# Kernel tuning notes

Hardware: AMD Instinct MI355X
Metric: run time of the kernel (lower is better)

## Reference

```python
import jax, jax.numpy as jnp
import numpy as np

D = 20                 # input_dim
N = 1_000_000          # batch
NC = 2 ** (D + 1)      # number of dummy expert Linear(1,1) modules


def setup_inputs() -> dict:
    key = jax.random.key(0)
    ks = jax.random.split(key, 12)
    x = jax.random.randint(ks[0], (N, D), 0, 2).astype(jnp.float32)   # binary features
    t = jax.random.randint(ks[1], (N, 1), 0, 2).astype(jnp.float32)   # binary treatment
    y = jax.random.normal(ks[2], (N, 1), dtype=jnp.float32)           # outcome fed to dummy linears
    # Encoder dummy experts: one (w, b) pair per combination of (t, x)
    qz_w = jax.random.normal(ks[3], (NC,), dtype=jnp.float32) * 0.1
    qz_b = jax.random.normal(ks[4], (NC,), dtype=jnp.float32) * 0.1
    # Decoder per-feature Linear(1,1) for binary x
    dx_w = jax.random.normal(ks[5], (D,), dtype=jnp.float32) * 0.1
    dx_b = jax.random.normal(ks[6], (D,), dtype=jnp.float32) * 0.1
    # Decoder scalar Linear(1,1) heads
    t_w = jax.random.normal(ks[7], (), dtype=jnp.float32) * 0.1
    t_b = jnp.zeros((), jnp.float32)
    y0_w = jax.random.normal(ks[8], (), dtype=jnp.float32) * 0.1
    y0_b = jnp.zeros((), jnp.float32)
    y1_w = jax.random.normal(ks[9], (), dtype=jnp.float32) * 0.1
    y1_b = jnp.zeros((), jnp.float32)
    pz_logit = jnp.zeros((1,), jnp.float32)
    return {"x": x, "t": t, "y": y, "qz_w": qz_w, "qz_b": qz_b,
            "dx_w": dx_w, "dx_b": dx_b, "t_w": t_w, "t_b": t_b,
            "y0_w": y0_w, "y0_b": y0_b, "y1_w": y1_w, "y1_b": y1_b,
            "pz_logit": pz_logit}


def _combo_index(x, t):
    # itertools.product([0,1], repeat=D+1): combs[i][0] is the t bit (MSB),
    # combs[i][1:] are the x bits, so i = t*2^D + sum_j x_j * 2^(D-1-j).
    pow2 = (2 ** jnp.arange(D - 1, -1, -1)).astype(jnp.int32)   # [D]
    return t[:, 0].astype(jnp.int32) * (2 ** D) + x.astype(jnp.int32) @ pow2  # [N]


def _decode(z, t, dx_w, dx_b, t_w, t_b, y0_w, y0_b, y1_w, y1_b):
    # Vectorized form of per-feature Linear(1,1) loops: x_logits[:, i] = w_i*z + b_i
    x_logits = z * dx_w[None, :] + dx_b[None, :]          # [N, D]
    t_logits = z * t_w + t_b                              # [N, 1]
    y_logits = (z * y1_w + y1_b) * t + (z * y0_w + y0_b) * (1.0 - t)  # [N, 1]
    return x_logits, t_logits, y_logits


def reference(x, t, y, qz_w, qz_b, dx_w, dx_b, t_w, t_b,
              y0_w, y0_b, y1_w, y1_b, pz_logit):
    # Encoder (z_mode='binary'): sum over all 2^(D+1) experts of
    # (w_i*y + b_i) * onehot_mask_i == gather by combination index (inputs binary).
    idx = _combo_index(x, t)                                  # [N]
    z_logits = (qz_w[idx] * y[:, 0] + qz_b[idx])[:, None]     # [N, 1]
    n = x.shape[0]
    z0 = jnp.zeros((n, 1), jnp.float32)
    z1 = jnp.ones((n, 1), jnp.float32)
    x_logits0, t_logits0, y_logits0 = _decode(z0, t, dx_w, dx_b, t_w, t_b, y0_w, y0_b, y1_w, y1_b)
    x_logits1, t_logits1, y_logits1 = _decode(z1, t, dx_w, dx_b, t_w, t_b, y0_w, y0_b, y1_w, y1_b)
    return (z_logits, x_logits0, x_logits1, t_logits0, t_logits1,
            y_logits0, y_logits1, pz_logit)
```

## Files before the change

kernel.cpp:

```cpp
#include <hip/hip_runtime.h>

constexpr int D = 20;

typedef float f4 __attribute__((ext_vector_type(4)));
typedef unsigned int u32;

__device__ __forceinline__ u32 bf16_rne(float f) {
    u32 u = __float_as_uint(f);
    return (u + 0x7FFFu + ((u >> 16) & 1u)) >> 16;
}

__global__ __launch_bounds__(256) void cevae_build_tab(
    const f4* __restrict__ qw, const f4* __restrict__ qb,
    uint4* __restrict__ tab, int nq)
{
    int i = blockIdx.x * 256 + threadIdx.x;
    if (i >= nq) return;
    f4 w = qw[i];
    f4 b = qb[i];
    uint4 o;
    o.x = (bf16_rne(w.x) << 16) | bf16_rne(b.x);
    o.y = (bf16_rne(w.y) << 16) | bf16_rne(b.y);
    o.z = (bf16_rne(w.z) << 16) | bf16_rne(b.z);
    o.w = (bf16_rne(w.w) << 16) | bf16_rne(b.w);
    tab[i] = o;
}

template <bool USE_TAB>
__global__ __launch_bounds__(256) void cevae_fused7_kernel(
    const float* __restrict__ x, const float* __restrict__ t,
    const float* __restrict__ y, const u32* __restrict__ tab,
    const float* __restrict__ qz_w, const float* __restrict__ qz_b,
    const float* __restrict__ dx_w, const float* __restrict__ dx_b,
    const float* __restrict__ sc_tw, const float* __restrict__ sc_tb,
    const float* __restrict__ sc_y0w, const float* __restrict__ sc_y0b,
    const float* __restrict__ sc_y1w, const float* __restrict__ sc_y1b,
    const float* __restrict__ pz, float* __restrict__ out, int n_rows,
    int n_job_blocks)
{
    int bid = blockIdx.x;
    int sub = ((bid >> 4) << 3) | (bid & 7);
    size_t o3 = (size_t)n_rows * (size_t)(1 + 2 * D);

    if (((bid >> 3) & 1) == 0) {
        int n = sub * 256 + threadIdx.x;
        if (n >= n_rows) return;

        const f4* xr = (const f4*)(x + (size_t)n * D);
        f4 a = xr[0];
        f4 b = xr[1];
        f4 c = xr[2];
        f4 d = xr[3];
        f4 e = xr[4];
        float tv = t[n];
        float yv = y[n];

        unsigned idx = (tv != 0.0f) ? (1u << 20) : 0u;
        idx |= ((unsigned)a.x) << 19;
        idx |= ((unsigned)a.y) << 18;
        idx |= ((unsigned)a.z) << 17;
        idx |= ((unsigned)a.w) << 16;
        idx |= ((unsigned)b.x) << 15;
        idx |= ((unsigned)b.y) << 14;
        idx |= ((unsigned)b.z) << 13;
        idx |= ((unsigned)b.w) << 12;
        idx |= ((unsigned)c.x) << 11;
        idx |= ((unsigned)c.y) << 10;
        idx |= ((unsigned)c.z) << 9;
        idx |= ((unsigned)c.w) << 8;
        idx |= ((unsigned)d.x) << 7;
        idx |= ((unsigned)d.y) << 6;
        idx |= ((unsigned)d.z) << 5;
        idx |= ((unsigned)d.w) << 4;
        idx |= ((unsigned)e.x) << 3;
        idx |= ((unsigned)e.y) << 2;
        idx |= ((unsigned)e.z) << 1;
        idx |= ((unsigned)e.w);

        float z;
        if (USE_TAB) {
            u32 g = tab[idx];
            z = fmaf(__uint_as_float(g & 0xFFFF0000u), yv,
                     __uint_as_float(g << 16));
        } else {
            z = fmaf(qz_w[idx], yv, qz_b[idx]);
        }
        out[n] = z;

        float y0w = *sc_y0w, y0b = *sc_y0b;
        float y1w = *sc_y1w, y1b = *sc_y1b;

        out[o3 + 2 * (size_t)n_rows + n] = fmaf(tv, y1b - y0b, y0b);
        out[o3 + 3 * (size_t)n_rows + n] = fmaf(tv, (y1w + y1b) - (y0w + y0b), y0w + y0b);
        if (n == 0) out[o3 + 4 * (size_t)n_rows] = pz[0];
    } else {
        unsigned Q = (unsigned)n_rows * D / 4;
        f4* r0 = (f4*)(out + n_rows);
        f4* r1 = r0 + Q;
        unsigned stride = (unsigned)n_job_blocks * 256;
        unsigned q0 = (unsigned)sub * 256 + threadIdx.x;
        for (unsigned q = q0; q < Q; q += stride) {
            int cb = (int)(q % 5u) * 4;
            float b0 = dx_b[cb + 0], b1 = dx_b[cb + 1];
            float b2 = dx_b[cb + 2], b3 = dx_b[cb + 3];
            float w0 = dx_w[cb + 0], w1 = dx_w[cb + 1];
            float w2 = dx_w[cb + 2], w3 = dx_w[cb + 3];
            f4 v0 = {b0, b1, b2, b3};
            f4 v1 = {w0 + b0, w1 + b1, w2 + b2, w3 + b3};
            __builtin_nontemporal_store(v0, r0 + q);
            __builtin_nontemporal_store(v1, r1 + q);
        }
        float tw = *sc_tw, tb = *sc_tb;
        f4 s0 = {tb, tb, tb, tb};
        float t1v = tw + tb;
        f4 s1 = {t1v, t1v, t1v, t1v};
        unsigned Qt = (unsigned)n_rows / 4;
        f4* h0 = (f4*)(out + o3);
        f4* h1 = (f4*)(out + o3 + (size_t)n_rows);
        for (unsigned q = q0; q < Qt; q += stride) {
            __builtin_nontemporal_store(s0, h0 + q);
            __builtin_nontemporal_store(s1, h1 + q);
        }
    }
}

extern "C" void kernel_launch(void* const* d_in, const int* in_sizes, int n_in,
                              void* d_out, int out_size, void* d_ws, size_t ws_size,
                              hipStream_t stream) {
    const float* x    = (const float*)d_in[0];
    const float* t    = (const float*)d_in[1];
    const float* y    = (const float*)d_in[2];
    const float* qz_w = (const float*)d_in[3];
    const float* qz_b = (const float*)d_in[4];
    const float* dx_w = (const float*)d_in[5];
    const float* dx_b = (const float*)d_in[6];
    const float* t_w  = (const float*)d_in[7];
    const float* t_b  = (const float*)d_in[8];
    const float* y0_w = (const float*)d_in[9];
    const float* y0_b = (const float*)d_in[10];
    const float* y1_w = (const float*)d_in[11];
    const float* y1_b = (const float*)d_in[12];
    const float* pz   = (const float*)d_in[13];
    float* out = (float*)d_out;

    int n_rows = in_sizes[0] / D;
    int nc     = in_sizes[3];
    int n_rb = (n_rows + 255) / 256;
    int n_groups = (n_rb + 7) / 8;
    int n_job_blocks = n_groups * 8;

    size_t tab_bytes = (size_t)nc * sizeof(u32);
    if (ws_size >= tab_bytes) {
        uint4* tab = (uint4*)d_ws;
        int nq = nc / 4;
        cevae_build_tab<<<(nq + 255) / 256, 256, 0, stream>>>(
            (const f4*)qz_w, (const f4*)qz_b, tab, nq);
        cevae_fused7_kernel<true><<<n_groups * 16, 256, 0, stream>>>(
            x, t, y, (const u32*)tab, qz_w, qz_b, dx_w, dx_b, t_w, t_b,
            y0_w, y0_b, y1_w, y1_b, pz, out, n_rows, n_job_blocks);
    } else {
        cevae_fused7_kernel<false><<<n_groups * 16, 256, 0, stream>>>(
            x, t, y, nullptr, qz_w, qz_b, dx_w, dx_b, t_w, t_b,
            y0_w, y0_b, y1_w, y1_b, pz, out, n_rows, n_job_blocks);
    }
}
```

Baseline: 66.09 us.

## Process four rows per thread and rebalance gather versus fill block split

Each gather thread now handles four rows spaced a quarter of the batch apart, which puts four independent table lookups in flight per thread to raise memory-level parallelism. The block interleave changes from 1:1 to 1:3 gather to fill groups, so the fill side gets three times as many blocks while the gather side gets a quarter as many threads. The rows handled by one thread sit far apart in memory, so coalescing still comes from adjacent threads. The fewer gather threads may expose latency if four-way ILP is not enough, and the remainder rows when n_rows is not a multiple of 4 are not handled.

```diff
diff --git a/kernel.cpp b/kernel.cpp
--- a/kernel.cpp
+++ b/kernel.cpp
@@ -26,8 +26,24 @@
     tab[i] = o;
 }
 
+__device__ __forceinline__ u32 combo_idx(const f4* xr, float tv) {
+    f4 a = xr[0], b = xr[1], c = xr[2], d = xr[3], e = xr[4];
+    u32 id = (tv != 0.0f) ? (1u << 20) : 0u;
+    id |= ((u32)a.x) << 19; id |= ((u32)a.y) << 18;
+    id |= ((u32)a.z) << 17; id |= ((u32)a.w) << 16;
+    id |= ((u32)b.x) << 15; id |= ((u32)b.y) << 14;
+    id |= ((u32)b.z) << 13; id |= ((u32)b.w) << 12;
+    id |= ((u32)c.x) << 11; id |= ((u32)c.y) << 10;
+    id |= ((u32)c.z) << 9;  id |= ((u32)c.w) << 8;
+    id |= ((u32)d.x) << 7;  id |= ((u32)d.y) << 6;
+    id |= ((u32)d.z) << 5;  id |= ((u32)d.w) << 4;
+    id |= ((u32)e.x) << 3;  id |= ((u32)e.y) << 2;
+    id |= ((u32)e.z) << 1;  id |= ((u32)e.w);
+    return id;
+}
+
 template <bool USE_TAB>
-__global__ __launch_bounds__(256) void cevae_fused7_kernel(
+__global__ __launch_bounds__(256) void cevae_fused8_kernel(
     const float* __restrict__ x, const float* __restrict__ t,
     const float* __restrict__ y, const u32* __restrict__ tab,
     const float* __restrict__ qz_w, const float* __restrict__ qz_b,
@@ -36,69 +52,69 @@
     const float* __restrict__ sc_y0w, const float* __restrict__ sc_y0b,
     const float* __restrict__ sc_y1w, const float* __restrict__ sc_y1b,
     const float* __restrict__ pz, float* __restrict__ out, int n_rows,
-    int n_job_blocks)
+    int n_fill_blocks)
 {
     int bid = blockIdx.x;
-    int sub = ((bid >> 4) << 3) | (bid & 7);
+    int g = bid >> 3;
     size_t o3 = (size_t)n_rows * (size_t)(1 + 2 * D);
 
-    if (((bid >> 3) & 1) == 0) {
-        int n = sub * 256 + threadIdx.x;
-        if (n >= n_rows) return;
+    if ((g & 3) == 0) {
+        int sub = (g >> 2) * 8 + (bid & 7);
+        int Qr = n_rows >> 2;
+        int m = sub * 256 + threadIdx.x;
+        if (m >= Qr) return;
 
-        const f4* xr = (const f4*)(x + (size_t)n * D);
-        f4 a = xr[0];
-        f4 b = xr[1];
-        f4 c = xr[2];
-        f4 d = xr[3];
-        f4 e = xr[4];
-        float tv = t[n];
-        float yv = y[n];
+        int n0 = m, n1 = m + Qr, n2 = m + 2 * Qr, n3 = m + 3 * Qr;
 
-        unsigned idx = (tv != 0.0f) ? (1u << 20) : 0u;
-        idx |= ((unsigned)a.x) << 19;
-        idx |= ((unsigned)a.y) << 18;
-        idx |= ((unsigned)a.z) << 17;
-        idx |= ((unsigned)a.w) << 16;
-        idx |= ((unsigned)b.x) << 15;
-        idx |= ((unsigned)b.y) << 14;
-        idx |= ((unsigned)b.z) << 13;
-        idx |= ((unsigned)b.w) << 12;
-        idx |= ((unsigned)c.x) << 11;
-        idx |= ((unsigned)c.y) << 10;
-        idx |= ((unsigned)c.z) << 9;
-        idx |= ((unsigned)c.w) << 8;
-        idx |= ((unsigned)d.x) << 7;
-        idx |= ((unsigned)d.y) << 6;
-        idx |= ((unsigned)d.z) << 5;
-        idx |= ((unsigned)d.w) << 4;
-        idx |= ((unsigned)e.x) << 3;
-        idx |= ((unsigned)e.y) << 2;
-        idx |= ((unsigned)e.z) << 1;
-        idx |= ((unsigned)e.w);
+        float t0 = t[n0], t1 = t[n1], t2 = t[n2], t3 = t[n3];
+        u32 i0 = combo_idx((const f4*)(x + (size_t)n0 * D), t0);
+        u32 i1 = combo_idx((const f4*)(x + (size_t)n1 * D), t1);
+        u32 i2 = combo_idx((const f4*)(x + (size_t)n2 * D), t2);
+        u32 i3 = combo_idx((const f4*)(x + (size_t)n3 * D), t3);
 
-        float z;
+        float y0v = y[n0], y1v = y[n1], y2v = y[n2], y3v = y[n3];
+
+        float z0, z1, z2, z3;
         if (USE_TAB) {
-            u32 g = tab[idx];
-            z = fmaf(__uint_as_float(g & 0xFFFF0000u), yv,
-                     __uint_as_float(g << 16));
+            u32 g0 = tab[i0], g1 = tab[i1], g2 = tab[i2], g3 = tab[i3];
+            z0 = fmaf(__uint_as_float(g0 & 0xFFFF0000u), y0v, __uint_as_float(g0 << 16));
+            z1 = fmaf(__uint_as_float(g1 & 0xFFFF0000u), y1v, __uint_as_float(g1 << 16));
+            z2 = fmaf(__uint_as_float(g2 & 0xFFFF0000u), y2v, __uint_as_float(g2 << 16));
+            z3 = fmaf(__uint_as_float(g3 & 0xFFFF0000u), y3v, __uint_as_float(g3 << 16));
         } else {
-            z = fmaf(qz_w[idx], yv, qz_b[idx]);
+            z0 = fmaf(qz_w[i0], y0v, qz_b[i0]);
+            z1 = fmaf(qz_w[i1], y1v, qz_b[i1]);
+            z2 = fmaf(qz_w[i2], y2v, qz_b[i2]);
+            z3 = fmaf(qz_w[i3], y3v, qz_b[i3]);
         }
-        out[n] = z;
+        out[n0] = z0;
+        out[n1] = z1;
+        out[n2] = z2;
+        out[n3] = z3;
 
         float y0w = *sc_y0w, y0b = *sc_y0b;
         float y1w = *sc_y1w, y1b = *sc_y1b;
+        float dy0 = y1b - y0b;
+        float dy1 = (y1w + y1b) - (y0w + y0b), c1 = y0w + y0b;
 
-        out[o3 + 2 * (size_t)n_rows + n] = fmaf(tv, y1b - y0b, y0b);
-        out[o3 + 3 * (size_t)n_rows + n] = fmaf(tv, (y1w + y1b) - (y0w + y0b), y0w + y0b);
-        if (n == 0) out[o3 + 4 * (size_t)n_rows] = pz[0];
+        float* yl0 = out + o3 + 2 * (size_t)n_rows;
+        float* yl1 = out + o3 + 3 * (size_t)n_rows;
+        yl0[n0] = fmaf(t0, dy0, y0b);
+        yl0[n1] = fmaf(t1, dy0, y0b);
+        yl0[n2] = fmaf(t2, dy0, y0b);
+        yl0[n3] = fmaf(t3, dy0, y0b);
+        yl1[n0] = fmaf(t0, dy1, c1);
+        yl1[n1] = fmaf(t1, dy1, c1);
+        yl1[n2] = fmaf(t2, dy1, c1);
+        yl1[n3] = fmaf(t3, dy1, c1);
+        if (m == 0) out[o3 + 4 * (size_t)n_rows] = pz[0];
     } else {
+        int fsub = (g - (g >> 2) - 1) * 8 + (bid & 7);
         unsigned Q = (unsigned)n_rows * D / 4;
         f4* r0 = (f4*)(out + n_rows);
         f4* r1 = r0 + Q;
-        unsigned stride = (unsigned)n_job_blocks * 256;
-        unsigned q0 = (unsigned)sub * 256 + threadIdx.x;
+        unsigned stride = (unsigned)n_fill_blocks * 256;
+        unsigned q0 = (unsigned)fsub * 256 + threadIdx.x;
         for (unsigned q = q0; q < Q; q += stride) {
             int cb = (int)(q % 5u) * 4;
             float b0 = dx_b[cb + 0], b1 = dx_b[cb + 1];
@@ -145,9 +161,12 @@
 
     int n_rows = in_sizes[0] / D;
     int nc     = in_sizes[3];
-    int n_rb = (n_rows + 255) / 256;
-    int n_groups = (n_rb + 7) / 8;
-    int n_job_blocks = n_groups * 8;
+
+    int Qr = n_rows / 4;
+    int n_rows_blocks = (Qr + 255) / 256;
+    int n_rows_groups = (n_rows_blocks + 7) / 8;
+    int n_groups = n_rows_groups * 4;
+    int n_fill_blocks = (n_groups - n_rows_groups) * 8;
 
     size_t tab_bytes = (size_t)nc * sizeof(u32);
     if (ws_size >= tab_bytes) {
@@ -155,12 +174,12 @@
         int nq = nc / 4;
         cevae_build_tab<<<(nq + 255) / 256, 256, 0, stream>>>(
             (const f4*)qz_w, (const f4*)qz_b, tab, nq);
-        cevae_fused7_kernel<true><<<n_groups * 16, 256, 0, stream>>>(
+        cevae_fused8_kernel<true><<<n_groups * 8, 256, 0, stream>>>(
             x, t, y, (const u32*)tab, qz_w, qz_b, dx_w, dx_b, t_w, t_b,
-            y0_w, y0_b, y1_w, y1_b, pz, out, n_rows, n_job_blocks);
+            y0_w, y0_b, y1_w, y1_b, pz, out, n_rows, n_fill_blocks);
     } else {
-        cevae_fused7_kernel<false><<<n_groups * 16, 256, 0, stream>>>(
+        cevae_fused8_kernel<false><<<n_groups * 8, 256, 0, stream>>>(
             x, t, y, nullptr, qz_w, qz_b, dx_w, dx_b, t_w, t_b,
-            y0_w, y0_b, y1_w, y1_b, pz, out, n_rows, n_job_blocks);
+            y0_w, y0_b, y1_w, y1_b, pz, out, n_rows, n_fill_blocks);
     }
 }
```

Measured after the change: 81.32 us. 1.23x slower.

## Merge gather and broadcast-store roles into every block to overlap latency

Applied to the files above, without the earlier changes.

Stops splitting blocks into separate gather and constant-store roles. Every thread now issues its x/t/y loads and table gather first, then runs the broadcast x_logits/t_logits store loops while those loads are in flight, and only then computes and writes z and y_logits. The aim is to hide gather latency behind the bulk streaming stores and halve the grid size. The remaining per-row scalar stores also become nontemporal. The cost is that each thread keeps its gather result in registers across the store loops, and all blocks now do mixed work.

```diff
diff --git a/kernel.cpp b/kernel.cpp
--- a/kernel.cpp
+++ b/kernel.cpp
@@ -27,7 +27,7 @@
 }
 
 template <bool USE_TAB>
-__global__ __launch_bounds__(256) void cevae_fused7_kernel(
+__global__ __launch_bounds__(256) void cevae_fused10_kernel(
     const float* __restrict__ x, const float* __restrict__ t,
     const float* __restrict__ y, const u32* __restrict__ tab,
     const float* __restrict__ qz_w, const float* __restrict__ qz_b,
@@ -35,27 +35,25 @@
     const float* __restrict__ sc_tw, const float* __restrict__ sc_tb,
     const float* __restrict__ sc_y0w, const float* __restrict__ sc_y0b,
     const float* __restrict__ sc_y1w, const float* __restrict__ sc_y1b,
-    const float* __restrict__ pz, float* __restrict__ out, int n_rows,
-    int n_job_blocks)
+    const float* __restrict__ pz, float* __restrict__ out, int n_rows)
 {
-    int bid = blockIdx.x;
-    int sub = ((bid >> 4) << 3) | (bid & 7);
+    int n = blockIdx.x * 256 + threadIdx.x;
     size_t o3 = (size_t)n_rows * (size_t)(1 + 2 * D);
+    unsigned stride = (unsigned)gridDim.x * 256u;
 
-    if (((bid >> 3) & 1) == 0) {
-        int n = sub * 256 + threadIdx.x;
-        if (n >= n_rows) return;
-
+    bool live = (n < n_rows);
+    float tv = 0.0f, yv = 0.0f;
+    unsigned idx = 0;
+    if (live) {
         const f4* xr = (const f4*)(x + (size_t)n * D);
         f4 a = xr[0];
         f4 b = xr[1];
         f4 c = xr[2];
         f4 d = xr[3];
         f4 e = xr[4];
-        float tv = t[n];
-        float yv = y[n];
-
-        unsigned idx = (tv != 0.0f) ? (1u << 20) : 0u;
+        tv = t[n];
+        yv = y[n];
+        idx = (tv != 0.0f) ? (1u << 20) : 0u;
         idx |= ((unsigned)a.x) << 19;
         idx |= ((unsigned)a.y) << 18;
         idx |= ((unsigned)a.z) << 17;
@@ -76,29 +74,24 @@
         idx |= ((unsigned)e.y) << 2;
         idx |= ((unsigned)e.z) << 1;
         idx |= ((unsigned)e.w);
+    }
 
-        float z;
+    u32 g = 0;
+    float gw = 0.0f, gb = 0.0f;
+    if (live) {
         if (USE_TAB) {
-            u32 g = tab[idx];
-            z = fmaf(__uint_as_float(g & 0xFFFF0000u), yv,
-                     __uint_as_float(g << 16));
+            g = tab[idx];
         } else {
-            z = fmaf(qz_w[idx], yv, qz_b[idx]);
+            gw = qz_w[idx];
+            gb = qz_b[idx];
         }
-        out[n] = z;
+    }
 
-        float y0w = *sc_y0w, y0b = *sc_y0b;
-        float y1w = *sc_y1w, y1b = *sc_y1b;
-
-        out[o3 + 2 * (size_t)n_rows + n] = fmaf(tv, y1b - y0b, y0b);
-        out[o3 + 3 * (size_t)n_rows + n] = fmaf(tv, (y1w + y1b) - (y0w + y0b), y0w + y0b);
-        if (n == 0) out[o3 + 4 * (size_t)n_rows] = pz[0];
-    } else {
+    {
         unsigned Q = (unsigned)n_rows * D / 4;
         f4* r0 = (f4*)(out + n_rows);
         f4* r1 = r0 + Q;
-        unsigned stride = (unsigned)n_job_blocks * 256;
-        unsigned q0 = (unsigned)sub * 256 + threadIdx.x;
+        unsigned q0 = (unsigned)blockIdx.x * 256u + threadIdx.x;
         for (unsigned q = q0; q < Q; q += stride) {
             int cb = (int)(q % 5u) * 4;
             float b0 = dx_b[cb + 0], b1 = dx_b[cb + 1];
@@ -121,6 +114,24 @@
             __builtin_nontemporal_store(s0, h0 + q);
             __builtin_nontemporal_store(s1, h1 + q);
         }
+    }
+
+    if (live) {
+        float y0w = *sc_y0w, y0b = *sc_y0b;
+        float y1w = *sc_y1w, y1b = *sc_y1b;
+        __builtin_nontemporal_store(fmaf(tv, y1b - y0b, y0b),
+                                    out + o3 + 2 * (size_t)n_rows + n);
+        __builtin_nontemporal_store(fmaf(tv, (y1w + y1b) - (y0w + y0b), y0w + y0b),
+                                    out + o3 + 3 * (size_t)n_rows + n);
+        float z;
+        if (USE_TAB) {
+            z = fmaf(__uint_as_float(g & 0xFFFF0000u), yv,
+                     __uint_as_float(g << 16));
+        } else {
+            z = fmaf(gw, yv, gb);
+        }
+        __builtin_nontemporal_store(z, out + n);
+        if (n == 0) out[o3 + 4 * (size_t)n_rows] = pz[0];
     }
 }
 
@@ -145,9 +156,8 @@
 
     int n_rows = in_sizes[0] / D;
     int nc     = in_sizes[3];
-    int n_rb = (n_rows + 255) / 256;
-    int n_groups = (n_rb + 7) / 8;
-    int n_job_blocks = n_groups * 8;
+    int n_blocks = (n_rows + 255) / 256;
+    n_blocks = ((n_blocks + 7) / 8) * 8;
 
     size_t tab_bytes = (size_t)nc * sizeof(u32);
     if (ws_size >= tab_bytes) {
@@ -155,12 +165,12 @@
         int nq = nc / 4;
         cevae_build_tab<<<(nq + 255) / 256, 256, 0, stream>>>(
             (const f4*)qz_w, (const f4*)qz_b, tab, nq);
-        cevae_fused7_kernel<true><<<n_groups * 16, 256, 0, stream>>>(
+        cevae_fused10_kernel<true><<<n_blocks, 256, 0, stream>>>(
             x, t, y, (const u32*)tab, qz_w, qz_b, dx_w, dx_b, t_w, t_b,
-            y0_w, y0_b, y1_w, y1_b, pz, out, n_rows, n_job_blocks);
+            y0_w, y0_b, y1_w, y1_b, pz, out, n_rows);
     } else {
-        cevae_fused7_kernel<false><<<n_groups * 16, 256, 0, stream>>>(
+        cevae_fused10_kernel<false><<<n_blocks, 256, 0, stream>>>(
             x, t, y, nullptr, qz_w, qz_b, dx_w, dx_b, t_w, t_b,
-            y0_w, y0_b, y1_w, y1_b, pz, out, n_rows, n_job_blocks);
+            y0_w, y0_b, y1_w, y1_b, pz, out, n_rows);
     }
 }
```

Result: no change. 65.56 us (-0.8%).
